# Optimization experiments

Hardware: AMD Instinct MI355X
Metric: run time of the kernel (lower is better)

The kernel has to match this reference:

```python
import jax, jax.numpy as jnp
import numpy as np

B, H, S, D = 2, 8, 4096, 64

def setup_inputs() -> dict:
    key = jax.random.key(0)
    kq, kk, kv = jax.random.split(key, 3)
    queries = jax.random.normal(kq, (B, H, S, D), dtype=jnp.float32)
    keys = jax.random.normal(kk, (B, H, S, D), dtype=jnp.float32)
    values = jax.random.normal(kv, (B, H, S, D), dtype=jnp.float32)
    adj = jnp.zeros((1,), dtype=jnp.int32)  # unused by the module, kept for signature fidelity
    return {"queries": queries, "keys": keys, "values": values, "adj": adj}

def reference(queries, keys, values, adj):
    # scores: [B,H,S,S]; note the original divides by a hard-coded 16, not sqrt(d)
    scores = jnp.einsum('bhqd,bhkd->bhqk', queries, keys) / 16.0
    attn = jax.nn.softmax(scores, axis=-1)
    # dropout p=0.0 -> identity in eval/deterministic mode
    h = jnp.einsum('bhqk,bhkd->bhqd', attn, values)  # [B,H,S,D]
    # original uses .view (a reshape, NOT a transpose) to (S, B, H, D)
    return jnp.reshape(h, (S, B, H, D))
```

## Files before the change

kernel.cpp:

```cpp
#include <hip/hip_runtime.h>
#include <hip/hip_bf16.h>
#include <math.h>

#define S_LEN 4096
#define D_DIM 64
#define NBH   16
#define NKT   64
#define QPRE  0.09016844f

typedef __attribute__((ext_vector_type(8))) short bf16x8;
typedef __attribute__((ext_vector_type(4))) float f32x4;
typedef __attribute__((ext_vector_type(16))) float f32x16;
typedef __attribute__((ext_vector_type(8))) __fp16 f16x8;
typedef __attribute__((ext_vector_type(2))) __fp16 f16x2;
typedef __attribute__((ext_vector_type(2))) unsigned int u32x2;

__device__ __forceinline__ unsigned int pkbf(float lo, float hi) {
  unsigned int ua = __float_as_uint(lo) + 0x8000u;
  unsigned int ub = __float_as_uint(hi) + 0x8000u;
  return __builtin_amdgcn_perm(ub, ua, 0x07060302u);
}
__device__ __forceinline__ unsigned int pkhf(float lo, float hi) {
  f16x2 h = __builtin_amdgcn_cvt_pkrtz(lo, hi);
  return *(unsigned int*)&h;
}
__device__ __forceinline__ void dma16(const unsigned short* g, unsigned short* l) {
  __builtin_amdgcn_global_load_lds(
      (const __attribute__((address_space(1))) unsigned int*)g,
      (__attribute__((address_space(3))) unsigned int*)l, 16, 0, 0);
}

__global__ __launch_bounds__(256) void prep(const float* __restrict__ K,
                                            const float* __restrict__ V,
                                            unsigned short* __restrict__ Kbf,
                                            unsigned short* __restrict__ Vt) {
  const int tid = threadIdx.x;
  __shared__ unsigned short tile[64][72];
  if (blockIdx.x < 256) {
    const int bh = blockIdx.x >> 4, ch = blockIdx.x & 15;
    const size_t base = ((size_t)bh * S_LEN + ch * 256) * D_DIM;
#pragma unroll
    for (int p = 0; p < 8; ++p) {
      int i = tid + p * 256;
      int row = i >> 3, c = (i & 7) * 8;
      float4 a = *(const float4*)&K[base + row * D_DIM + c];
      float4 b = *(const float4*)&K[base + row * D_DIM + c + 4];
      uint4 w;
      w.x = pkbf(a.x, a.y); w.y = pkbf(a.z, a.w);
      w.z = pkbf(b.x, b.y); w.w = pkbf(b.z, b.w);
      *(uint4*)&Kbf[base + row * D_DIM + c] = w;
    }
    return;
  }
  const int blk = blockIdx.x - 256;
  const int bh = blk >> 6, kt = blk & 63;
  const float* src = V + ((size_t)bh * S_LEN + kt * 64) * D_DIM;
#pragma unroll
  for (int p = 0; p < 4; ++p) {
    int i = tid + p * 256;
    int row = i >> 4, c = (i & 15) * 4;
    float4 f = *(const float4*)&src[row * D_DIM + c];
    int cs = c ^ (((row >> 4) & 3) << 4);
    unsigned long long w = (unsigned long long)pkhf(f.x, f.y) |
                           ((unsigned long long)pkhf(f.z, f.w) << 32);
    *(unsigned long long*)&tile[row][cs] = w;
  }
  __syncthreads();
  const int kc = tid & 7;
#pragma unroll
  for (int p = 0; p < 2; ++p) {
    int d = p * 32 + (tid >> 3);
    int col = d ^ (((kc >> 1) & 3) << 4);
    union { unsigned short u[8]; uint4 v; } t;
#pragma unroll
    for (int i = 0; i < 8; ++i) t.u[i] = tile[kc * 8 + i][col];
    *(uint4*)&Vt[((size_t)bh * D_DIM + d) * S_LEN + kt * 64 + kc * 8] = t.v;
  }
}

__global__ __launch_bounds__(256, 4) void fattn(const float* __restrict__ Q,
                                                const unsigned short* __restrict__ Kbf,
                                                const unsigned short* __restrict__ Vt,
                                                float* __restrict__ Of) {
  const int bh   = blockIdx.x & 15;
  const int qb   = blockIdx.x >> 4;
  const int tid  = threadIdx.x;
  const int wave = tid >> 6;
  const int lane = tid & 63;
  const int l31  = lane & 31;
  const int hi   = lane >> 5;

  __shared__ unsigned short Ksh[2][64][64];
  __shared__ unsigned short Vsh[2][64][64];

  bf16x8 qf2[4];
  {
    const int qg = qb * 128 + wave * 32 + l31;
    const float* qp = Q + ((size_t)bh * S_LEN + qg) * D_DIM + hi * 8;
#pragma unroll
    for (int dm = 0; dm < 4; ++dm) {
      float4 a = *(const float4*)&qp[dm * 16];
      float4 b = *(const float4*)&qp[dm * 16 + 4];
      union { unsigned int u[4]; bf16x8 v; } f;
      f.u[0] = pkbf(a.x * QPRE, a.y * QPRE);
      f.u[1] = pkbf(a.z * QPRE, a.w * QPRE);
      f.u[2] = pkbf(b.x * QPRE, b.y * QPRE);
      f.u[3] = pkbf(b.z * QPRE, b.w * QPRE);
      qf2[dm] = f.v;
    }
  }

  f32x16 ov[2] = {{}, {}};
  float Lt = 0.f;

  const unsigned short* Kb = Kbf + (size_t)bh * S_LEN * D_DIM;
  const unsigned short* Vb = Vt + (size_t)bh * D_DIM * S_LEN;

  const int r_lo = wave * 8 + (lane >> 3);
  const int csrc = ((lane & 7) ^ (lane >> 3)) * 8;

#define DMAK(T, B) do { const int t_ = (T); \
  dma16(&Kb[(size_t)(t_ * 64 + r_lo) * 64 + csrc],      &Ksh[B][wave * 8][0]); \
  dma16(&Kb[(size_t)(t_ * 64 + r_lo + 32) * 64 + csrc], &Ksh[B][wave * 8 + 32][0]); } while (0)
#define DMAV(T, B) do { const int t_ = (T); \
  dma16(&Vb[(size_t)r_lo * S_LEN + t_ * 64 + csrc],        &Vsh[B][wave * 8][0]); \
  dma16(&Vb[(size_t)(r_lo + 32) * S_LEN + t_ * 64 + csrc], &Vsh[B][wave * 8 + 32][0]); } while (0)

#define SCORES(KB, PD) do { \
  const char* kbase_ = (const char*)&Ksh[KB][0][0]; \
  _Pragma("unroll") \
  for (int kt2 = 0; kt2 < 2; ++kt2) { \
    const int krow_ = kt2 * 32 + l31; \
    f32x16 acc2 = {}; \
    _Pragma("unroll") \
    for (int dm = 0; dm < 4; ++dm) { \
      bf16x8 kf = *(const bf16x8*)(kbase_ + krow_ * 128 + (((dm * 2 + hi) ^ (krow_ & 7)) * 16)); \
      acc2 = __builtin_amdgcn_mfma_f32_32x32x16_bf16(kf, qf2[dm], acc2, 0, 0, 0); \
    } \
    float pp[16]; \
    _Pragma("unroll") \
    for (int j = 0; j < 16; ++j) pp[j] = __builtin_amdgcn_exp2f(acc2[j]); \
    Lt += (((pp[0] + pp[1]) + (pp[2] + pp[3])) + ((pp[4] + pp[5]) + (pp[6] + pp[7]))) \
        + (((pp[8] + pp[9]) + (pp[10] + pp[11])) + ((pp[12] + pp[13]) + (pp[14] + pp[15]))); \
    unsigned int w00 = pkhf(pp[0], pp[1]),   w01 = pkhf(pp[2], pp[3]); \
    unsigned int w10 = pkhf(pp[4], pp[5]),   w11 = pkhf(pp[6], pp[7]); \
    unsigned int w20 = pkhf(pp[8], pp[9]),   w21 = pkhf(pp[10], pp[11]); \
    unsigned int w30 = pkhf(pp[12], pp[13]), w31 = pkhf(pp[14], pp[15]); \
    u32x2 s0 = __builtin_amdgcn_permlane32_swap(w00, w10, false, false); \
    u32x2 s1 = __builtin_amdgcn_permlane32_swap(w01, w11, false, false); \
    u32x2 s2 = __builtin_amdgcn_permlane32_swap(w20, w30, false, false); \
    u32x2 s3 = __builtin_amdgcn_permlane32_swap(w21, w31, false, false); \
    PD[kt2 * 2 + 0][0] = s0.x; PD[kt2 * 2 + 0][1] = s1.x; \
    PD[kt2 * 2 + 0][2] = s0.y; PD[kt2 * 2 + 0][3] = s1.y; \
    PD[kt2 * 2 + 1][0] = s2.x; PD[kt2 * 2 + 1][1] = s3.x; \
    PD[kt2 * 2 + 1][2] = s2.y; PD[kt2 * 2 + 1][3] = s3.y; \
  } } while (0)

#define PVSTEP(VB, PU) do { \
  const char* vbase_ = (const char*)&Vsh[VB][0][0]; \
  _Pragma("unroll") \
  for (int dt2 = 0; dt2 < 2; ++dt2) { \
    const int drow_ = dt2 * 32 + l31; \
    _Pragma("unroll") \
    for (int s4 = 0; s4 < 4; ++s4) { \
      f16x8 va = *(const f16x8*)(vbase_ + drow_ * 128 + (((s4 * 2 + hi) ^ (drow_ & 7)) * 16)); \
      union { unsigned int u[4]; f16x8 v; } pb; \
      pb.u[0] = PU[s4][0]; pb.u[1] = PU[s4][1]; \
      pb.u[2] = PU[s4][2]; pb.u[3] = PU[s4][3]; \
      ov[dt2] = __builtin_amdgcn_mfma_f32_32x32x16_f16(va, pb.v, ov[dt2], 0, 0, 0); \
    } \
  } } while (0)

  unsigned int pA[4][4];

  DMAK(0, 0); DMAV(0, 0);
  __syncthreads();

  for (int b = 0; b < NKT - 2; b += 2) {
    DMAK(b + 1, 1); DMAV(b + 1, 1);
    SCORES(0, pA);
    PVSTEP(0, pA);
    __syncthreads();
    DMAK(b + 2, 0); DMAV(b + 2, 0);
    SCORES(1, pA);
    PVSTEP(1, pA);
    __syncthreads();
  }
  DMAK(NKT - 1, 1); DMAV(NKT - 1, 1);
  SCORES(0, pA);
  PVSTEP(0, pA);
  __syncthreads();
  SCORES(1, pA);
  PVSTEP(1, pA);

  Lt += __shfl_xor(Lt, 32);
  const float linv = 1.0f / Lt;
  const size_t grow = (size_t)bh * S_LEN + qb * 128 + wave * 32 + l31;
#pragma unroll
  for (int dt2 = 0; dt2 < 2; ++dt2)
#pragma unroll
    for (int m = 0; m < 4; ++m) {
      float4 w = {ov[dt2][4 * m + 0] * linv, ov[dt2][4 * m + 1] * linv,
                  ov[dt2][4 * m + 2] * linv, ov[dt2][4 * m + 3] * linv};
      *(float4*)&Of[grow * 64 + dt2 * 32 + m * 8 + hi * 4] = w;
    }
#undef DMAK
#undef DMAV
#undef SCORES
#undef PVSTEP
}

extern "C" void kernel_launch(void* const* d_in, const int* in_sizes, int n_in,
                              void* d_out, int out_size, void* d_ws, size_t ws_size,
                              hipStream_t stream) {
  const float* Q = (const float*)d_in[0];
  const float* K = (const float*)d_in[1];
  const float* V = (const float*)d_in[2];
  unsigned short* Kbf = (unsigned short*)d_ws;
  unsigned short* Vt  = Kbf + (size_t)NBH * S_LEN * D_DIM;
  float* Of = (float*)d_out;

  prep<<<1280, 256, 0, stream>>>(K, V, Kbf, Vt);
  fattn<<<NBH * 32, 256, 0, stream>>>(Q, Kbf, Vt, Of);
}
```

Measured before the change: 169.7 us.

## Split each key tile across two wave groups and reduce partial outputs in LDS

Doubles the block to 512 threads (8 waves). Each group of four waves handles one 32-key half of every 64-key tile for the same 128 queries, so each wave does half the score and PV work per tile. The 4 K-loading waves and 4 V-loading waves now issue their DMA copies separately. Partial outputs and row sums from the second half are merged through shared memory at the end, which adds an epilogue sync and LDS traffic. Register pressure and occupancy change under the 512-thread launch bound.

```diff
diff --git a/kernel.cpp b/kernel.cpp
--- a/kernel.cpp
+++ b/kernel.cpp
@@ -78,7 +78,7 @@
   }
 }
 
-__global__ __launch_bounds__(256, 4) void fattn(const float* __restrict__ Q,
+__global__ __launch_bounds__(512, 4) void fattn(const float* __restrict__ Q,
                                                 const unsigned short* __restrict__ Kbf,
                                                 const unsigned short* __restrict__ Vt,
                                                 float* __restrict__ Of) {
@@ -89,13 +89,16 @@
   const int lane = tid & 63;
   const int l31  = lane & 31;
   const int hi   = lane >> 5;
-
-  __shared__ unsigned short Ksh[2][64][64];
-  __shared__ unsigned short Vsh[2][64][64];
+  const int sq   = wave & 3;
+  const int kh   = wave >> 2;
+
+  __shared__ __align__(16) char smem[34816];
+  unsigned short (*Ksh)[64][64] = (unsigned short (*)[64][64])smem;
+  unsigned short (*Vsh)[64][64] = (unsigned short (*)[64][64])(smem + 16384);
 
   bf16x8 qf2[4];
   {
-    const int qg = qb * 128 + wave * 32 + l31;
+    const int qg = qb * 128 + sq * 32 + l31;
     const float* qp = Q + ((size_t)bh * S_LEN + qg) * D_DIM + hi * 8;
 #pragma unroll
     for (int dm = 0; dm < 4; ++dm) {
@@ -116,45 +119,43 @@
   const unsigned short* Kb = Kbf + (size_t)bh * S_LEN * D_DIM;
   const unsigned short* Vb = Vt + (size_t)bh * D_DIM * S_LEN;
 
-  const int r_lo = wave * 8 + (lane >> 3);
+  const int r8   = (wave & 3) * 8 + (lane >> 3);
   const int csrc = ((lane & 7) ^ (lane >> 3)) * 8;
-
-#define DMAK(T, B) do { const int t_ = (T); \
-  dma16(&Kb[(size_t)(t_ * 64 + r_lo) * 64 + csrc],      &Ksh[B][wave * 8][0]); \
-  dma16(&Kb[(size_t)(t_ * 64 + r_lo + 32) * 64 + csrc], &Ksh[B][wave * 8 + 32][0]); } while (0)
-#define DMAV(T, B) do { const int t_ = (T); \
-  dma16(&Vb[(size_t)r_lo * S_LEN + t_ * 64 + csrc],        &Vsh[B][wave * 8][0]); \
-  dma16(&Vb[(size_t)(r_lo + 32) * S_LEN + t_ * 64 + csrc], &Vsh[B][wave * 8 + 32][0]); } while (0)
+  const int rx7  = l31 & 7;
+  const int krow = kh * 32 + l31;
+
+#define STAGE(T, B) do { const int t_ = (T); \
+  if (wave < 4) { \
+    dma16(&Kb[(size_t)(t_ * 64 + r8) * 64 + csrc],      &Ksh[B][(wave & 3) * 8][0]); \
+    dma16(&Kb[(size_t)(t_ * 64 + r8 + 32) * 64 + csrc], &Ksh[B][(wave & 3) * 8 + 32][0]); \
+  } else { \
+    dma16(&Vb[(size_t)r8 * S_LEN + t_ * 64 + csrc],        &Vsh[B][(wave & 3) * 8][0]); \
+    dma16(&Vb[(size_t)(r8 + 32) * S_LEN + t_ * 64 + csrc], &Vsh[B][(wave & 3) * 8 + 32][0]); \
+  } } while (0)
 
 #define SCORES(KB, PD) do { \
   const char* kbase_ = (const char*)&Ksh[KB][0][0]; \
+  f32x16 acc2 = {}; \
   _Pragma("unroll") \
-  for (int kt2 = 0; kt2 < 2; ++kt2) { \
-    const int krow_ = kt2 * 32 + l31; \
-    f32x16 acc2 = {}; \
-    _Pragma("unroll") \
-    for (int dm = 0; dm < 4; ++dm) { \
-      bf16x8 kf = *(const bf16x8*)(kbase_ + krow_ * 128 + (((dm * 2 + hi) ^ (krow_ & 7)) * 16)); \
-      acc2 = __builtin_amdgcn_mfma_f32_32x32x16_bf16(kf, qf2[dm], acc2, 0, 0, 0); \
-    } \
-    float pp[16]; \
-    _Pragma("unroll") \
-    for (int j = 0; j < 16; ++j) pp[j] = __builtin_amdgcn_exp2f(acc2[j]); \
-    Lt += (((pp[0] + pp[1]) + (pp[2] + pp[3])) + ((pp[4] + pp[5]) + (pp[6] + pp[7]))) \
-        + (((pp[8] + pp[9]) + (pp[10] + pp[11])) + ((pp[12] + pp[13]) + (pp[14] + pp[15]))); \
-    unsigned int w00 = pkhf(pp[0], pp[1]),   w01 = pkhf(pp[2], pp[3]); \
-    unsigned int w10 = pkhf(pp[4], pp[5]),   w11 = pkhf(pp[6], pp[7]); \
-    unsigned int w20 = pkhf(pp[8], pp[9]),   w21 = pkhf(pp[10], pp[11]); \
-    unsigned int w30 = pkhf(pp[12], pp[13]), w31 = pkhf(pp[14], pp[15]); \
-    u32x2 s0 = __builtin_amdgcn_permlane32_swap(w00, w10, false, false); \
-    u32x2 s1 = __builtin_amdgcn_permlane32_swap(w01, w11, false, false); \
-    u32x2 s2 = __builtin_amdgcn_permlane32_swap(w20, w30, false, false); \
-    u32x2 s3 = __builtin_amdgcn_permlane32_swap(w21, w31, false, false); \
-    PD[kt2 * 2 + 0][0] = s0.x; PD[kt2 * 2 + 0][1] = s1.x; \
-    PD[kt2 * 2 + 0][2] = s0.y; PD[kt2 * 2 + 0][3] = s1.y; \
-    PD[kt2 * 2 + 1][0] = s2.x; PD[kt2 * 2 + 1][1] = s3.x; \
-    PD[kt2 * 2 + 1][2] = s2.y; PD[kt2 * 2 + 1][3] = s3.y; \
-  } } while (0)
+  for (int dm = 0; dm < 4; ++dm) { \
+    bf16x8 kf = *(const bf16x8*)(kbase_ + krow * 128 + (((dm * 2 + hi) ^ rx7) * 16)); \
+    acc2 = __builtin_amdgcn_mfma_f32_32x32x16_bf16(kf, qf2[dm], acc2, 0, 0, 0); \
+  } \
+  float pp[16]; \
+  _Pragma("unroll") \
+  for (int j = 0; j < 16; ++j) pp[j] = __builtin_amdgcn_exp2f(acc2[j]); \
+  Lt += (((pp[0] + pp[1]) + (pp[2] + pp[3])) + ((pp[4] + pp[5]) + (pp[6] + pp[7]))) \
+      + (((pp[8] + pp[9]) + (pp[10] + pp[11])) + ((pp[12] + pp[13]) + (pp[14] + pp[15]))); \
+  unsigned int w00 = pkhf(pp[0], pp[1]),   w01 = pkhf(pp[2], pp[3]); \
+  unsigned int w10 = pkhf(pp[4], pp[5]),   w11 = pkhf(pp[6], pp[7]); \
+  unsigned int w20 = pkhf(pp[8], pp[9]),   w21 = pkhf(pp[10], pp[11]); \
+  unsigned int w30 = pkhf(pp[12], pp[13]), w31 = pkhf(pp[14], pp[15]); \
+  u32x2 s0 = __builtin_amdgcn_permlane32_swap(w00, w10, false, false); \
+  u32x2 s1 = __builtin_amdgcn_permlane32_swap(w01, w11, false, false); \
+  u32x2 s2 = __builtin_amdgcn_permlane32_swap(w20, w30, false, false); \
+  u32x2 s3 = __builtin_amdgcn_permlane32_swap(w21, w31, false, false); \
+  PD[0][0] = s0.x; PD[0][1] = s1.x; PD[0][2] = s0.y; PD[0][3] = s1.y; \
+  PD[1][0] = s2.x; PD[1][1] = s3.x; PD[1][2] = s2.y; PD[1][3] = s3.y; } while (0)
 
 #define PVSTEP(VB, PU) do { \
   const char* vbase_ = (const char*)&Vsh[VB][0][0]; \
@@ -162,31 +163,32 @@
   for (int dt2 = 0; dt2 < 2; ++dt2) { \
     const int drow_ = dt2 * 32 + l31; \
     _Pragma("unroll") \
-    for (int s4 = 0; s4 < 4; ++s4) { \
-      f16x8 va = *(const f16x8*)(vbase_ + drow_ * 128 + (((s4 * 2 + hi) ^ (drow_ & 7)) * 16)); \
+    for (int s4l = 0; s4l < 2; ++s4l) { \
+      const int ck_ = (((kh * 2 + s4l) * 2 + hi) ^ rx7) * 16; \
+      f16x8 va = *(const f16x8*)(vbase_ + drow_ * 128 + ck_); \
       union { unsigned int u[4]; f16x8 v; } pb; \
-      pb.u[0] = PU[s4][0]; pb.u[1] = PU[s4][1]; \
-      pb.u[2] = PU[s4][2]; pb.u[3] = PU[s4][3]; \
+      pb.u[0] = PU[s4l][0]; pb.u[1] = PU[s4l][1]; \
+      pb.u[2] = PU[s4l][2]; pb.u[3] = PU[s4l][3]; \
       ov[dt2] = __builtin_amdgcn_mfma_f32_32x32x16_f16(va, pb.v, ov[dt2], 0, 0, 0); \
     } \
   } } while (0)
 
-  unsigned int pA[4][4];
-
-  DMAK(0, 0); DMAV(0, 0);
+  unsigned int pA[2][4];
+
+  STAGE(0, 0);
   __syncthreads();
 
   for (int b = 0; b < NKT - 2; b += 2) {
-    DMAK(b + 1, 1); DMAV(b + 1, 1);
+    STAGE(b + 1, 1);
     SCORES(0, pA);
     PVSTEP(0, pA);
     __syncthreads();
-    DMAK(b + 2, 0); DMAV(b + 2, 0);
+    STAGE(b + 2, 0);
     SCORES(1, pA);
     PVSTEP(1, pA);
     __syncthreads();
   }
-  DMAK(NKT - 1, 1); DMAV(NKT - 1, 1);
+  STAGE(NKT - 1, 1);
   SCORES(0, pA);
   PVSTEP(0, pA);
   __syncthreads();
@@ -194,18 +196,35 @@
   PVSTEP(1, pA);
 
   Lt += __shfl_xor(Lt, 32);
-  const float linv = 1.0f / Lt;
-  const size_t grow = (size_t)bh * S_LEN + qb * 128 + wave * 32 + l31;
-#pragma unroll
-  for (int dt2 = 0; dt2 < 2; ++dt2)
-#pragma unroll
-    for (int m = 0; m < 4; ++m) {
-      float4 w = {ov[dt2][4 * m + 0] * linv, ov[dt2][4 * m + 1] * linv,
-                  ov[dt2][4 * m + 2] * linv, ov[dt2][4 * m + 3] * linv};
-      *(float4*)&Of[grow * 64 + dt2 * 32 + m * 8 + hi * 4] = w;
-    }
-#undef DMAK
-#undef DMAV
+  __syncthreads();
+  float* sc = (float*)smem;
+  const int sbase = (sq * 64 + lane) * 33;
+  if (kh) {
+    sc[sbase + 32] = Lt;
+#pragma unroll
+    for (int j = 0; j < 16; ++j) sc[sbase + j] = ov[0][j];
+#pragma unroll
+    for (int j = 0; j < 16; ++j) sc[sbase + 16 + j] = ov[1][j];
+  }
+  __syncthreads();
+  if (!kh) {
+    Lt += sc[sbase + 32];
+#pragma unroll
+    for (int j = 0; j < 16; ++j) ov[0][j] += sc[sbase + j];
+#pragma unroll
+    for (int j = 0; j < 16; ++j) ov[1][j] += sc[sbase + 16 + j];
+    const float linv = 1.0f / Lt;
+    const size_t grow = (size_t)bh * S_LEN + qb * 128 + sq * 32 + l31;
+#pragma unroll
+    for (int dt2 = 0; dt2 < 2; ++dt2)
+#pragma unroll
+      for (int m = 0; m < 4; ++m) {
+        float4 w = {ov[dt2][4 * m + 0] * linv, ov[dt2][4 * m + 1] * linv,
+                    ov[dt2][4 * m + 2] * linv, ov[dt2][4 * m + 3] * linv};
+        *(float4*)&Of[grow * 64 + dt2 * 32 + m * 8 + hi * 4] = w;
+      }
+  }
+#undef STAGE
 #undef SCORES
 #undef PVSTEP
 }
@@ -221,5 +240,5 @@
   float* Of = (float*)d_out;
 
   prep<<<1280, 256, 0, stream>>>(K, V, Kbf, Vt);
-  fattn<<<NBH * 32, 256, 0, stream>>>(Q, Kbf, Vt, Of);
-}
+  fattn<<<NBH * 32, 512, 0, stream>>>(Q, Kbf, Vt, Of);
+}
```

New measurement: 167.3 us. About the same (-1.5%).
